# Kernel tuning notes

Hardware: AMD Instinct MI355X
Metric: run time of the kernel (lower is better)

The kernel has to match this reference:

```python
import jax, jax.numpy as jnp
import numpy as np

N, H, W, C = 128, 256, 256, 3
P = 1.0
XFLIP = 1.0
YFLIP = 1.0
ROTATE_INT = 1.0
TRANSLATE_INT = 1.0
TRANSLATE_INT_MAX = 0.125


def setup_inputs() -> dict:
    key = jax.random.key(0)
    ks = jax.random.split(key, 9)
    return {
        'images': jax.random.normal(ks[0], (N, H, W, C), dtype=jnp.float32),
        'xflip_w': jax.random.randint(ks[1], (N, 1, 1, 1), 0, 2, dtype=jnp.int32),
        'xflip_gate': jax.random.uniform(ks[2], (N, 1, 1, 1), dtype=jnp.float32),
        'yflip_w': jax.random.randint(ks[3], (N, 1, 1, 1), 0, 2, dtype=jnp.int32),
        'yflip_gate': jax.random.uniform(ks[4], (N, 1, 1, 1), dtype=jnp.float32),
        'rot_w': jax.random.randint(ks[5], (N, 1, 1, 1), 0, 4, dtype=jnp.int32),
        'rot_gate': jax.random.uniform(ks[6], (N, 1, 1, 1), dtype=jnp.float32),
        'trans_w': jax.random.uniform(ks[7], (2, N, 1, 1, 1), dtype=jnp.float32),
        'trans_gate': jax.random.uniform(ks[8], (1, N, 1, 1, 1), dtype=jnp.float32),
    }


def _augment(images, xflip_w, xflip_gate, yflip_w, yflip_gate, rot_w, rot_gate,
             trans_w, trans_gate):
    n, h, w_, c = images.shape

    # --- x-flip (per-sample gated horizontal flip) ---
    wv = jnp.where(xflip_gate < XFLIP * P, xflip_w, jnp.zeros_like(xflip_w))
    images = jnp.where(wv == 1, jnp.flip(images, 2), images)

    # --- y-flip ---
    wv = jnp.where(yflip_gate < YFLIP * P, yflip_w, jnp.zeros_like(yflip_w))
    images = jnp.where(wv == 1, jnp.flip(images, 1), images)

    # --- 90-degree rotations (requires H == W) ---
    wv = jnp.where(rot_gate < ROTATE_INT * P, rot_w, jnp.zeros_like(rot_w))
    images = jnp.where((wv == 1) | (wv == 2), jnp.flip(images, 2), images)
    images = jnp.where((wv == 2) | (wv == 3), jnp.flip(images, 1), images)
    images = jnp.where((wv == 1) | (wv == 3), jnp.transpose(images, (0, 2, 1, 3)), images)

    # --- integer translation with reflection padding (gather) ---
    tw = trans_w * 2.0 - 1.0                                   # [2,N,1,1,1] in [-1,1)
    tw = jnp.where(trans_gate < TRANSLATE_INT * P, tw, jnp.zeros_like(tw))
    tx = jnp.round(tw[0] * w_ * TRANSLATE_INT_MAX).astype(jnp.int32)[:, 0, 0, 0]  # [N]
    ty = jnp.round(tw[1] * h * TRANSLATE_INT_MAX).astype(jnp.int32)[:, 0, 0, 0]   # [N]
    tx = jax.lax.stop_gradient(tx)
    ty = jax.lax.stop_gradient(ty)
    # reflected source indices per sample: [N, W] and [N, H]
    xi = w_ - 1 - jnp.abs(w_ - 1 - (jnp.arange(w_)[None, :] - tx[:, None]) % (w_ * 2 - 2))
    yi = h - 1 - jnp.abs(h - 1 - (jnp.arange(h)[None, :] + ty[:, None]) % (h * 2 - 2))
    images = jax.vmap(lambda im, y, x: im[y][:, x])(images, yi, xi)
    return images


def reference(images, xflip_w, xflip_gate, yflip_w, yflip_gate, rot_w, rot_gate,
              trans_w, trans_gate):
    return _augment(images, xflip_w, xflip_gate, yflip_w, yflip_gate,
                    rot_w, rot_gate, trans_w, trans_gate)
```

## Files before the change

### kernel.cpp

```cpp
#include <hip/hip_runtime.h>

#define NN 128
#define HH 256
#define WW 256
#define CC 3
#define HWC (HH * WW * CC)
#define TILE 32
#define LSTRIDE 99

__device__ __forceinline__ int reflect_idx(int v, int size) {
    int period = 2 * size - 2;
    int m = v % period;
    if (m < 0) m += period;
    return size - 1 - abs(size - 1 - m);
}

__global__ __launch_bounds__(256) void augment_kernel(
    const float* __restrict__ images,
    const int*   __restrict__ xflip_w,
    const float* __restrict__ xflip_gate,
    const int*   __restrict__ yflip_w,
    const float* __restrict__ yflip_gate,
    const int*   __restrict__ rot_w,
    const float* __restrict__ rot_gate,
    const float* __restrict__ trans_w,
    const float* __restrict__ trans_gate,
    float* __restrict__ out)
{
    __shared__ int   sy_arr[TILE];
    __shared__ int   sx_arr[TILE];
    __shared__ float tile[TILE * LSTRIDE];

    const int n       = blockIdx.x >> 6;
    const int tile_id = blockIdx.x & 63;
    const int yo0     = (tile_id >> 3) << 5;
    const int xo0     = (tile_id & 7) << 5;

    const bool xf = (xflip_gate[n] < 1.0f) && (xflip_w[n] == 1);
    const bool yf = (yflip_gate[n] < 1.0f) && (yflip_w[n] == 1);
    const int  rw = (rot_gate[n] < 1.0f) ? rot_w[n] : 0;
    const bool fx = ((rw == 1) || (rw == 2)) ^ xf;
    const bool fy = ((rw == 2) || (rw == 3)) ^ yf;
    const bool tr = (rw == 1) || (rw == 3);

    float tw0 = trans_w[n]      * 2.0f - 1.0f;
    float tw1 = trans_w[NN + n] * 2.0f - 1.0f;
    if (!(trans_gate[n] < 1.0f)) { tw0 = 0.0f; tw1 = 0.0f; }
    const int tx = (int)rintf(tw0 * (WW * 0.125f));
    const int ty = (int)rintf(tw1 * (HH * 0.125f));

    if (threadIdx.x < 64) {
        const int t = threadIdx.x & 31;
        if (threadIdx.x < 32) {
            int v = tr ? reflect_idx(xo0 + t - tx, WW)
                       : reflect_idx(yo0 + t + ty, HH);
            if (fy) v = HH - 1 - v;
            sy_arr[t] = v;
        } else {
            int v = tr ? reflect_idx(yo0 + t + ty, HH)
                       : reflect_idx(xo0 + t - tx, WW);
            if (fx) v = WW - 1 - v;
            sx_arr[t] = v;
        }
    }
    __syncthreads();

    const float* __restrict__ src = images + (size_t)n * HWC;

    if (!tr) {
        for (int t = threadIdx.x; t < TILE * TILE * CC; t += 256) {
            const int i = t / 96;
            const int k = t - i * 96;
            const int j = k / 3;
            const int c = k - j * 3;
            const float v = src[(sy_arr[i] * WW + sx_arr[j]) * CC + c];
            out[((size_t)(n * HH + yo0 + i)) * (WW * CC) + xo0 * CC + k] = v;
        }
    } else {
        for (int t = threadIdx.x; t < TILE * TILE * CC; t += 256) {
            const int j = t / 96;
            const int k = t - j * 96;
            const int i = k / 3;
            const int c = k - i * 3;
            tile[i * LSTRIDE + j * 3 + c] =
                src[(sy_arr[j] * WW + sx_arr[i]) * CC + c];
        }
        __syncthreads();
        for (int t = threadIdx.x; t < TILE * TILE * CC; t += 256) {
            const int i = t / 96;
            const int k = t - i * 96;
            out[((size_t)(n * HH + yo0 + i)) * (WW * CC) + xo0 * CC + k] =
                tile[i * LSTRIDE + k];
        }
    }
}

extern "C" void kernel_launch(void* const* d_in, const int* in_sizes, int n_in,
                              void* d_out, int out_size, void* d_ws, size_t ws_size,
                              hipStream_t stream)
{
    const float* images     = (const float*)d_in[0];
    const int*   xflip_w    = (const int*)  d_in[1];
    const float* xflip_gate = (const float*)d_in[2];
    const int*   yflip_w    = (const int*)  d_in[3];
    const float* yflip_gate = (const float*)d_in[4];
    const int*   rot_w      = (const int*)  d_in[5];
    const float* rot_gate   = (const float*)d_in[6];
    const float* trans_w    = (const float*)d_in[7];
    const float* trans_gate = (const float*)d_in[8];
    float* outp = (float*)d_out;

    dim3 grid(NN * 64);
    dim3 block(256);
    augment_kernel<<<grid, block, 0, stream>>>(images, xflip_w, xflip_gate,
                                               yflip_w, yflip_gate, rot_w, rot_gate,
                                               trans_w, trans_gate, outp);
}
```

Baseline: 41.76 us.

## Stage contiguous source rows via float4 loads into LDS and vectorize output stores

Each tile now checks whether its 32 reflected source columns form a contiguous range. If they do, it loads whole aligned row windows with float4 reads into shared memory, and otherwise falls back to a per-element gather. Every tile, transposed or not, now goes through shared memory and is written out with float4 stores, using a precomputed column-remap table. The aim is fewer scalar global memory transactions, paid for with extra syncs, a serial min/max scan by one thread, and some wasted loads from over-fetching the window.

```diff
diff --git a/kernel.cpp b/kernel.cpp
--- a/kernel.cpp
+++ b/kernel.cpp
@@ -5,8 +5,9 @@
 #define WW 256
 #define CC 3
 #define HWC (HH * WW * CC)
-#define TILE 32
-#define LSTRIDE 99
+#define ROWF (WW * CC)
+#define LSF 100
+#define WIN 100
 
 __device__ __forceinline__ int reflect_idx(int v, int size) {
     int period = 2 * size - 2;
@@ -27,9 +28,11 @@
     const float* __restrict__ trans_gate,
     float* __restrict__ out)
 {
-    __shared__ int   sy_arr[TILE];
-    __shared__ int   sx_arr[TILE];
-    __shared__ float tile[TILE * LSTRIDE];
+    __shared__ __align__(16) float ldsf[32 * LSF];
+    __shared__ __align__(16) int   syv768[32];
+    __shared__ __align__(16) int   sxr[32];
+    __shared__ __align__(16) int   rc[96];
+    __shared__ int info[2];
 
     const int n       = blockIdx.x >> 6;
     const int tile_id = blockIdx.x & 63;
@@ -49,49 +52,103 @@
     const int tx = (int)rintf(tw0 * (WW * 0.125f));
     const int ty = (int)rintf(tw1 * (HH * 0.125f));
 
-    if (threadIdx.x < 64) {
-        const int t = threadIdx.x & 31;
-        if (threadIdx.x < 32) {
+    {
+        const int t = threadIdx.x;
+        if (t < 32) {
             int v = tr ? reflect_idx(xo0 + t - tx, WW)
                        : reflect_idx(yo0 + t + ty, HH);
             if (fy) v = HH - 1 - v;
-            sy_arr[t] = v;
-        } else {
-            int v = tr ? reflect_idx(yo0 + t + ty, HH)
-                       : reflect_idx(xo0 + t - tx, WW);
+            syv768[t] = v * ROWF;
+        } else if (t < 64) {
+            const int u = t - 32;
+            int v = tr ? reflect_idx(yo0 + u + ty, HH)
+                       : reflect_idx(xo0 + u - tx, WW);
             if (fx) v = WW - 1 - v;
-            sx_arr[t] = v;
+            sxr[u] = v;
         }
+    }
+    __syncthreads();
+    if (threadIdx.x == 0) {
+        int mn = sxr[0], mx = sxr[0];
+        #pragma unroll
+        for (int u = 1; u < 32; ++u) {
+            const int v = sxr[u];
+            mn = min(mn, v); mx = max(mx, v);
+        }
+        info[0] = (mx - mn == 31);
+        info[1] = mn;
+    }
+    __syncthreads();
+    const int fast = info[0];
+    const int mn   = info[1];
+    const int base_f = mn * 3;
+    const int align4 = min(base_f & ~3, ROWF - WIN);
+    const int shift  = base_f - align4;
+
+    if (threadIdx.x < 96) {
+        const int m  = threadIdx.x;
+        const int jm = (m * 171) >> 9;
+        const int cm = m - 3 * jm;
+        rc[m] = fast ? ((sxr[jm] - mn) * 3 + cm + shift) : m;
     }
     __syncthreads();
 
     const float* __restrict__ src = images + (size_t)n * HWC;
 
-    if (!tr) {
-        for (int t = threadIdx.x; t < TILE * TILE * CC; t += 256) {
-            const int i = t / 96;
-            const int k = t - i * 96;
-            const int j = k / 3;
-            const int c = k - j * 3;
-            const float v = src[(sy_arr[i] * WW + sx_arr[j]) * CC + c];
-            out[((size_t)(n * HH + yo0 + i)) * (WW * CC) + xo0 * CC + k] = v;
+    if (fast) {
+        float4* lds4 = (float4*)ldsf;
+        #pragma unroll
+        for (int v = 0; v < 4; ++v) {
+            const int f = threadIdx.x + v * 256;
+            if (f < 800) {
+                const int row = (f * 1311) >> 15;
+                const int q   = f - row * 25;
+                const float4* srow = (const float4*)(src + syv768[row] + align4);
+                lds4[row * 25 + q] = srow[q];
+            }
         }
     } else {
-        for (int t = threadIdx.x; t < TILE * TILE * CC; t += 256) {
-            const int j = t / 96;
-            const int k = t - j * 96;
-            const int i = k / 3;
-            const int c = k - i * 3;
-            tile[i * LSTRIDE + j * 3 + c] =
-                src[(sy_arr[j] * WW + sx_arr[i]) * CC + c];
+        #pragma unroll
+        for (int v = 0; v < 12; ++v) {
+            const int f   = threadIdx.x + v * 256;
+            const int j5  = f >> 5;
+            const int row = (j5 * 171) >> 9;
+            const int m   = f - row * 96;
+            const int jm  = (m * 171) >> 9;
+            const int cm  = m - 3 * jm;
+            ldsf[row * LSF + m] = src[syv768[row] + sxr[jm] * 3 + cm];
         }
-        __syncthreads();
-        for (int t = threadIdx.x; t < TILE * TILE * CC; t += 256) {
-            const int i = t / 96;
-            const int k = t - i * 96;
-            out[((size_t)(n * HH + yo0 + i)) * (WW * CC) + xo0 * CC + k] =
-                tile[i * LSTRIDE + k];
+    }
+    __syncthreads();
+
+    const size_t outBase4 = (size_t)(n * HH + yo0) * (ROWF / 4) + ((xo0 * 3) >> 2);
+    float4* __restrict__ out4 = (float4*)out;
+    const int4* rc4 = (const int4*)rc;
+
+    #pragma unroll
+    for (int v = 0; v < 3; ++v) {
+        const int q4 = threadIdx.x + v * 256;
+        const int i  = (q4 * 683) >> 14;
+        const int q2 = q4 - i * 24;
+        float4 o;
+        if (!tr) {
+            const int4 r = rc4[q2];
+            const float* lrow = ldsf + i * LSF;
+            o.x = lrow[r.x]; o.y = lrow[r.y]; o.z = lrow[r.z]; o.w = lrow[r.w];
+        } else {
+            const int rci0 = rc[i * 3 + 0];
+            const int rci1 = rc[i * 3 + 1];
+            const int rci2 = rc[i * 3 + 2];
+            #pragma unroll
+            for (int u = 0; u < 4; ++u) {
+                const int k2 = 4 * q2 + u;
+                const int j  = (k2 * 171) >> 9;
+                const int c  = k2 - 3 * j;
+                const int rcv = (c == 0) ? rci0 : ((c == 1) ? rci1 : rci2);
+                ((float*)&o)[u] = ldsf[j * LSF + rcv];
+            }
         }
+        out4[outBase4 + (size_t)i * (ROWF / 4) + q2] = o;
     }
 }
 
```

Result: faster. 39.33 us (-5.8%).
